# Performance work log

Measured on AMD Instinct MI355X. Metric: run time of the kernel, lower is better.

## Reference

```python
import jax, jax.numpy as jnp
import numpy as np

B, IMG, P, S, D, H, HD = 64, 224, 16, 197, 768, 12, 64
MLP, L, PRUNE_AFTER, NCLS = 3072, 12, 4, 1000
N_KEEP = max(1, int(S * 0.5))  # FIXED_RATIO = 0.5 -> 98 kept tokens (plus forced CLS)


def _ln(x, w, b, eps=1e-6):
    m = x.mean(-1, keepdims=True)
    v = ((x - m) ** 2).mean(-1, keepdims=True)
    return (x - m) * jax.lax.rsqrt(v + eps) * w + b


def _block(x, ln1_w, ln1_b, qkv_w, qkv_b, proj_w, proj_b,
           ln2_w, ln2_b, fc1_w, fc1_b, fc2_w, fc2_b, key_mask=None):
    b, s, _ = x.shape
    qkv = _ln(x, ln1_w, ln1_b) @ qkv_w.T + qkv_b           # [B,S,3D]
    qkv = qkv.reshape(b, s, 3, H, HD)
    q, k, v = qkv[:, :, 0], qkv[:, :, 1], qkv[:, :, 2]     # [B,S,H,HD]
    logits = jnp.einsum('bqhd,bkhd->bhqk', q * (HD ** -0.5), k)
    if key_mask is not None:
        # masking pruned keys == varlen attention restricted to kept tokens
        logits = jnp.where(key_mask[:, None, None, :], logits, -1e9)
    attn = jax.nn.softmax(logits, axis=-1)
    out = jnp.einsum('bhqk,bkhd->bqhd', attn, v).reshape(b, s, D)
    x = x + out @ proj_w.T + proj_b
    h = _ln(x, ln2_w, ln2_b)
    h = jax.nn.gelu(h @ fc1_w.T + fc1_b, approximate=False) @ fc2_w.T + fc2_b
    return x + h


def _forward(images, patch_w, patch_b, cls_token, pos_embed,
             ln1_w, ln1_b, qkv_w, qkv_b, proj_w, proj_b,
             ln2_w, ln2_b, fc1_w, fc1_b, fc2_w, fc2_b,
             norm_w, norm_b, head_w, head_b):
    # patch embed: conv stride P == non-overlapping patch projection
    x = jax.lax.conv_general_dilated(images, patch_w, (P, P), 'VALID',
                                     dimension_numbers=('NCHW', 'OIHW', 'NCHW'))
    x = x.reshape(x.shape[0], D, -1).transpose(0, 2, 1) + patch_b       # [B,196,D]
    x = jnp.concatenate([jnp.broadcast_to(cls_token, (x.shape[0], 1, D)), x], axis=1)
    x = x + pos_embed                                                    # [B,197,D]
    for i in range(PRUNE_AFTER):
        x = _block(x, ln1_w[i], ln1_b[i], qkv_w[i], qkv_b[i], proj_w[i], proj_b[i],
                   ln2_w[i], ln2_b[i], fc1_w[i], fc1_b[i], fc2_w[i], fc2_b[i])
    # norm-score topk prune (CLS always kept), as in _threshold_prune
    scores = jnp.linalg.norm(x, axis=-1)                                 # [B,S]
    _, idx = jax.lax.top_k(scores, N_KEEP)
    mask = jnp.zeros((x.shape[0], S), bool)
    mask = mask.at[jnp.arange(x.shape[0])[:, None], idx].set(True).at[:, 0].set(True)
    # Padded-mask form of triton_pack_tokens + flash_attn_varlen: pruned tokens
    # are never attended to (masked keys) and their own outputs are unused.
    for i in range(PRUNE_AFTER, L):
        x = _block(x, ln1_w[i], ln1_b[i], qkv_w[i], qkv_b[i], proj_w[i], proj_b[i],
                   ln2_w[i], ln2_b[i], fc1_w[i], fc1_b[i], fc2_w[i], fc2_b[i],
                   key_mask=mask)
    cls = _ln(x[:, 0], norm_w, norm_b)   # packed[cu[:-1]] is always the CLS token
    return cls @ head_w.T + head_b       # [B, NCLS]


def setup_inputs():
    key = jax.random.key(0)
    ks = iter(jax.random.split(key, 32))
    def rn(shape, s=0.02):
        return jax.random.normal(next(ks), shape, jnp.float32) * s
    return {
        'images': jax.random.normal(next(ks), (B, 3, IMG, IMG), jnp.float32),
        'patch_w': rn((D, 3, P, P)), 'patch_b': jnp.zeros((D,), jnp.float32),
        'cls_token': rn((1, 1, D)), 'pos_embed': rn((1, S, D)),
        'ln1_w': jnp.ones((L, D), jnp.float32), 'ln1_b': jnp.zeros((L, D), jnp.float32),
        'qkv_w': rn((L, 3 * D, D)), 'qkv_b': jnp.zeros((L, 3 * D), jnp.float32),
        'proj_w': rn((L, D, D)), 'proj_b': jnp.zeros((L, D), jnp.float32),
        'ln2_w': jnp.ones((L, D), jnp.float32), 'ln2_b': jnp.zeros((L, D), jnp.float32),
        'fc1_w': rn((L, MLP, D)), 'fc1_b': jnp.zeros((L, MLP), jnp.float32),
        'fc2_w': rn((L, D, MLP)), 'fc2_b': jnp.zeros((L, D), jnp.float32),
        'norm_w': jnp.ones((D,), jnp.float32), 'norm_b': jnp.zeros((D,), jnp.float32),
        'head_w': rn((NCLS, D)), 'head_b': jnp.zeros((NCLS,), jnp.float32),
    }


def reference(images, patch_w, patch_b, cls_token, pos_embed,
              ln1_w, ln1_b, qkv_w, qkv_b, proj_w, proj_b,
              ln2_w, ln2_b, fc1_w, fc1_b, fc2_w, fc2_b,
              norm_w, norm_b, head_w, head_b):
    return _forward(images, patch_w, patch_b, cls_token, pos_embed,
                    ln1_w, ln1_b, qkv_w, qkv_b, proj_w, proj_b,
                    ln2_w, ln2_b, fc1_w, fc1_b, fc2_w, fc2_b,
                    norm_w, norm_b, head_w, head_b)
```

## Files before the change

### kernel.cpp

```cpp
#include <hip/hip_runtime.h>
#include <hip/hip_bf16.h>
#include <cstdint>

#define NH 12
#define SQ 197
#define DIM 768
#define HDIM 64
#define BATCH 64
#define MTOK (BATCH*SQ)
#define MLPD 3072
#define NKEEP 98
#define CSLOT 100
#define MCTOK (BATCH*CSLOT)
#define VLDF 224
#define VLDC 128

typedef __attribute__((ext_vector_type(8))) short bf16x8;
typedef __attribute__((ext_vector_type(8))) unsigned short ushort8;
typedef __attribute__((ext_vector_type(4))) unsigned short ushort4v;
typedef __attribute__((ext_vector_type(4))) float floatx4;

__device__ __forceinline__ unsigned short f2bf(float f) {
  __hip_bfloat16 h = __float2bfloat16(f);
  return reinterpret_cast<unsigned short&>(h);
}

__device__ __forceinline__ float erf_fast(float x) {
  float ax = fabsf(x);
  float t = 1.f / (1.f + 0.3275911f * ax);
  float y = t * (0.254829592f + t * (-0.284496736f + t * (1.421413741f +
            t * (-1.453152027f + t * 1.061405429f))));
  float r = 1.f - y * __expf(-ax * ax);
  return copysignf(r, x);
}

__device__ __forceinline__ void gload16(const unsigned short* g, unsigned short* l) {
  __builtin_amdgcn_global_load_lds(
      (const __attribute__((address_space(1))) void*)g,
      (__attribute__((address_space(3))) void*)l, 16, 0, 0);
}

enum { EPI_PATCH = 0, EPI_QKV = 1, EPI_RESID = 2, EPI_GELU = 3, EPI_HEAD = 4, EPI_QKVC = 5 };

template<int EPI, bool CHK, int MR, int NR>
__device__ __forceinline__ void gemm_epilogue(
    floatx4 (&acc)[MR][NR], int m0, int n0, int wr, int wc, int l15, int l4,
    const float* __restrict__ bias, int M, int N,
    float* __restrict__ xresid, const float* __restrict__ pos,
    unsigned short* __restrict__ obf, unsigned short* __restrict__ qb,
    unsigned short* __restrict__ kb, unsigned short* __restrict__ vb,
    float* __restrict__ ofp)
{
#pragma unroll
  for (int mr = 0; mr < MR; ++mr) {
#pragma unroll
    for (int nr = 0; nr < NR; ++nr) {
#pragma unroll
      for (int j = 0; j < 4; ++j) {
        int m = m0 + wr + mr * 16 + l4 * 4 + j;
        int n = n0 + wc + nr * 16 + l15;
        if (CHK && (m >= M || n >= N)) continue;
        float val = acc[mr][nr][j] + bias[n];
        if constexpr (EPI == EPI_PATCH) {
          int b = m / 196, p = m - b * 196;
          xresid[(size_t)(b * SQ + 1 + p) * DIM + n] = val + pos[(1 + p) * DIM + n];
        } else if constexpr (EPI == EPI_QKV || EPI == EPI_QKVC) {
          constexpr int SR = (EPI == EPI_QKV) ? SQ : CSLOT;
          constexpr int VL = (EPI == EPI_QKV) ? VLDF : VLDC;
          int part = n / DIM; int within = n - part * DIM;
          int h = within >> 6, hd = within & 63;
          int b = m / SR, s = m - b * SR;
          if (part == 0)      qb[(((size_t)(b * NH + h)) * SR + s) * HDIM + hd] = f2bf(val * 0.125f);
          else if (part == 1) kb[(((size_t)(b * NH + h)) * SR + s) * HDIM + hd] = f2bf(val);
          else                vb[(((size_t)(b * NH + h)) * HDIM + hd) * VL + s] = f2bf(val);
        } else if constexpr (EPI == EPI_RESID) {
          xresid[(size_t)m * DIM + n] += val;
        } else if constexpr (EPI == EPI_GELU) {
          float g = 0.5f * val * (1.f + erf_fast(val * 0.70710678118654752f));
          obf[(size_t)m * MLPD + n] = f2bf(g);
        } else {
          ofp[(size_t)m * 1000 + n] = val;
        }
      }
    }
  }
}

template<int EPI>
__global__ __launch_bounds__(512, 1)
void gemm_bf256(const unsigned short* __restrict__ A, int lda,
                const unsigned short* __restrict__ Wb, int ldw,
                const float* __restrict__ bias,
                int M, int N, int K,
                float* __restrict__ xresid,
                const float* __restrict__ pos,
                unsigned short* __restrict__ obf,
                unsigned short* __restrict__ qb,
                unsigned short* __restrict__ kb,
                unsigned short* __restrict__ vb,
                float* __restrict__ ofp)
{
  __shared__ unsigned short As[2][256 * 64];
  __shared__ unsigned short Bs[2][256 * 64];
  const int tid = threadIdx.x;
  const int lane = tid & 63;
  const int w = tid >> 6;
  const int wr = (w >> 2) * 128;
  const int wc = (w & 3) * 64;

  const int gx = gridDim.x;
  const int nwg = gx * gridDim.y;
  const int orig = blockIdx.y * gx + blockIdx.x;
  const int q = nwg >> 3, r = nwg & 7;
  const int xcd = orig & 7, o8 = orig >> 3;
  const int wgid = ((xcd < r) ? xcd * (q + 1) : r * (q + 1) + (xcd - r) * q) + o8;
  const int bx = wgid % gx, by = wgid / gx;
  const int m0 = by * 256, n0 = bx * 256;
  const int l15 = lane & 15, l4 = lane >> 4;

  const int sub = lane & 7, rsub = lane >> 3;
  const int scol = ((sub ^ rsub) << 3);
  const bool isA = (w < 4);
  const unsigned short* gp[8];
  int ldst[8];
#pragma unroll
  for (int j = 0; j < 8; ++j) {
    int row = (w & 3) * 64 + j * 8 + rsub;
    if (isA) {
      int ra = m0 + row; if (ra > M - 1) ra = M - 1;
      gp[j] = A + (size_t)ra * lda + scol;
    } else {
      int rb = n0 + row; if (rb > N - 1) rb = N - 1;
      gp[j] = Wb + (size_t)rb * ldw + scol;
    }
    ldst[j] = ((w & 3) * 8 + j) * 512;
  }

  floatx4 acc[8][4];
#pragma unroll
  for (int i = 0; i < 8; ++i)
#pragma unroll
    for (int j = 0; j < 4; ++j) acc[i][j] = {0.f, 0.f, 0.f, 0.f};

  auto STAGE = [&](int buf, int kt) {
    unsigned short* base = isA ? &As[buf][0] : &Bs[buf][0];
#pragma unroll
    for (int j = 0; j < 8; ++j)
      gload16(gp[j] + kt, base + ldst[j]);
  };

  const int nk = K >> 6;
  STAGE(0, 0);
  int cur = 0;
  for (int ki = 0; ki < nk; ++ki) {
    if (ki + 1 < nk) {
      STAGE(cur ^ 1, (ki + 1) << 6);
      asm volatile("s_waitcnt vmcnt(8)" ::: "memory");
    } else {
      asm volatile("s_waitcnt vmcnt(0)" ::: "memory");
    }
    __builtin_amdgcn_sched_barrier(0);
    __builtin_amdgcn_s_barrier();
    const unsigned short* Ac = &As[cur][0];
    const unsigned short* Bc = &Bs[cur][0];
#pragma unroll
    for (int kk = 0; kk < 2; ++kk) {
      bf16x8 af[8], bfr[4];
#pragma unroll
      for (int mr = 0; mr < 8; ++mr) {
        int row = wr + mr * 16 + l15;
        int cs = (kk * 4 + l4) ^ (row & 7);
        af[mr] = *(const bf16x8*)&Ac[row * 64 + cs * 8];
      }
#pragma unroll
      for (int nr = 0; nr < 4; ++nr) {
        int row = wc + nr * 16 + l15;
        int cs = (kk * 4 + l4) ^ (row & 7);
        bfr[nr] = *(const bf16x8*)&Bc[row * 64 + cs * 8];
      }
#pragma unroll
      for (int mr = 0; mr < 8; ++mr)
#pragma unroll
        for (int nr = 0; nr < 4; ++nr)
          acc[mr][nr] = __builtin_amdgcn_mfma_f32_16x16x32_bf16(af[mr], bfr[nr], acc[mr][nr], 0, 0, 0);
    }
    __builtin_amdgcn_sched_barrier(0);
    __builtin_amdgcn_s_barrier();
    cur ^= 1;
  }
  if (m0 + 256 <= M && n0 + 256 <= N)
    gemm_epilogue<EPI, false, 8, 4>(acc, m0, n0, wr, wc, l15, l4, bias, M, N,
                                    xresid, pos, obf, qb, kb, vb, ofp);
  else
    gemm_epilogue<EPI, true, 8, 4>(acc, m0, n0, wr, wc, l15, l4, bias, M, N,
                                   xresid, pos, obf, qb, kb, vb, ofp);
}

template<int EPI, int BN>
__global__ __launch_bounds__(256)
void gemm_bf(const unsigned short* __restrict__ A, int lda,
             const unsigned short* __restrict__ Wb, int ldw,
             const float* __restrict__ bias,
             int M, int N, int K,
             float* __restrict__ xresid,
             const float* __restrict__ pos,
             unsigned short* __restrict__ obf,
             unsigned short* __restrict__ qb,
             unsigned short* __restrict__ kb,
             unsigned short* __restrict__ vb,
             float* __restrict__ ofp)
{
  constexpr int NR = BN / 32;
  constexpr int NG = (128 + BN) / 8;
  constexpr int PG = NG / 4;
  __shared__ unsigned short As[128 * 64];
  __shared__ unsigned short Bs[BN * 64];
  const int tid = threadIdx.x;
  const int lane = tid & 63;
  const int w = tid >> 6;
  const int wr = (w >> 1) * 64, wc = (w & 1) * (BN / 2);

  const int gx = gridDim.x;
  const int nwg = gx * gridDim.y;
  const int orig = blockIdx.y * gx + blockIdx.x;
  const int q = nwg >> 3, r = nwg & 7;
  const int xcd = orig & 7, o8 = orig >> 3;
  const int wgid = ((xcd < r) ? xcd * (q + 1) : r * (q + 1) + (xcd - r) * q) + o8;
  const int bx = wgid % gx, by = wgid / gx;
  const int m0 = by * 128, n0 = bx * BN;
  const int l15 = lane & 15, l4 = lane >> 4;

  const int sub = lane & 7, rsub = lane >> 3;
  const int scol = ((sub ^ rsub) << 3);
  const unsigned short* gp[PG];
  unsigned short* lp[PG];
#pragma unroll
  for (int j = 0; j < PG; ++j) {
    int t = w * PG + j;
    if (t < 16) {
      int row = t * 8 + rsub;
      int ra = m0 + row; if (ra > M - 1) ra = M - 1;
      gp[j] = A + (size_t)ra * lda + scol;
      lp[j] = &As[t * 512];
    } else {
      int tb = t - 16;
      int row = tb * 8 + rsub;
      int rb = n0 + row; if (rb > N - 1) rb = N - 1;
      gp[j] = Wb + (size_t)rb * ldw + scol;
      lp[j] = &Bs[tb * 512];
    }
  }

  floatx4 acc[4][NR];
#pragma unroll
  for (int i = 0; i < 4; ++i)
#pragma unroll
    for (int j = 0; j < NR; ++j) acc[i][j] = {0.f, 0.f, 0.f, 0.f};

  for (int kt = 0; kt < K; kt += 64) {
#pragma unroll
    for (int j = 0; j < PG; ++j)
      gload16(gp[j] + kt, lp[j]);
    __syncthreads();
#pragma unroll
    for (int kk = 0; kk < 2; ++kk) {
      bf16x8 af[4], bfr[NR];
#pragma unroll
      for (int mr = 0; mr < 4; ++mr) {
        int row = wr + mr * 16 + l15;
        int cs = (kk * 4 + l4) ^ (row & 7);
        af[mr] = *(const bf16x8*)&As[row * 64 + cs * 8];
      }
#pragma unroll
      for (int nr = 0; nr < NR; ++nr) {
        int row = wc + nr * 16 + l15;
        int cs = (kk * 4 + l4) ^ (row & 7);
        bfr[nr] = *(const bf16x8*)&Bs[row * 64 + cs * 8];
      }
#pragma unroll
      for (int mr = 0; mr < 4; ++mr)
#pragma unroll
        for (int nr = 0; nr < NR; ++nr)
          acc[mr][nr] = __builtin_amdgcn_mfma_f32_16x16x32_bf16(af[mr], bfr[nr], acc[mr][nr], 0, 0, 0);
    }
    __syncthreads();
  }
  if (m0 + 128 <= M && n0 + BN <= N)
    gemm_epilogue<EPI, false, 4, NR>(acc, m0, n0, wr, wc, l15, l4, bias, M, N,
                                     xresid, pos, obf, qb, kb, vb, ofp);
  else
    gemm_epilogue<EPI, true, 4, NR>(acc, m0, n0, wr, wc, l15, l4, bias, M, N,
                                    xresid, pos, obf, qb, kb, vb, ofp);
}

template<int EPI>
__global__ __launch_bounds__(256)
void gemm_f32(const unsigned short* __restrict__ A, int lda,
              const float* __restrict__ Wf, int ldw,
              const float* __restrict__ bias,
              int M, int N, int K,
              float* __restrict__ xresid,
              const float* __restrict__ pos,
              unsigned short* __restrict__ obf,
              unsigned short* __restrict__ qb,
              unsigned short* __restrict__ kb,
              unsigned short* __restrict__ vb,
              float* __restrict__ ofp)
{
  __shared__ unsigned short As[128 * 64];
  __shared__ unsigned short Bs[128 * 64];
  const int tid = threadIdx.x;
  const int lane = tid & 63;
  const int w = tid >> 6;
  const int wr = (w >> 1) * 64, wc = (w & 1) * 64;
  const int m0 = blockIdx.y * 128, n0 = blockIdx.x * 128;
  const int l15 = lane & 15, l4 = lane >> 4;

  floatx4 acc[4][4];
#pragma unroll
  for (int i = 0; i < 4; ++i)
#pragma unroll
    for (int j = 0; j < 4; ++j) acc[i][j] = {0.f, 0.f, 0.f, 0.f};

  for (int kt = 0; kt < K; kt += 64) {
#pragma unroll
    for (int i = 0; i < 4; ++i) {
      int g = tid + 256 * i;
      int row = g >> 3, c = g & 7;
      int sw = (c ^ (row & 7)) * 8;
      int ra = m0 + row; if (ra > M - 1) ra = M - 1;
      ushort8 av = *(const ushort8*)(A + (size_t)ra * lda + kt + c * 8);
      *(ushort8*)&As[row * 64 + sw] = av;
      int rb = n0 + row; if (rb > N - 1) rb = N - 1;
      const float* bs = Wf + (size_t)rb * ldw + kt + c * 8;
      float4 f0 = *(const float4*)bs;
      float4 f1 = *(const float4*)(bs + 4);
      ushort8 bv;
      bv[0] = f2bf(f0.x); bv[1] = f2bf(f0.y); bv[2] = f2bf(f0.z); bv[3] = f2bf(f0.w);
      bv[4] = f2bf(f1.x); bv[5] = f2bf(f1.y); bv[6] = f2bf(f1.z); bv[7] = f2bf(f1.w);
      *(ushort8*)&Bs[row * 64 + sw] = bv;
    }
    __syncthreads();
#pragma unroll
    for (int kk = 0; kk < 2; ++kk) {
      bf16x8 af[4], bfr[4];
#pragma unroll
      for (int mr = 0; mr < 4; ++mr) {
        int row = wr + mr * 16 + l15;
        int cs = (kk * 4 + l4) ^ (row & 7);
        af[mr] = *(const bf16x8*)&As[row * 64 + cs * 8];
      }
#pragma unroll
      for (int nr = 0; nr < 4; ++nr) {
        int row = wc + nr * 16 + l15;
        int cs = (kk * 4 + l4) ^ (row & 7);
        bfr[nr] = *(const bf16x8*)&Bs[row * 64 + cs * 8];
      }
#pragma unroll
      for (int mr = 0; mr < 4; ++mr)
#pragma unroll
        for (int nr = 0; nr < 4; ++nr)
          acc[mr][nr] = __builtin_amdgcn_mfma_f32_16x16x32_bf16(af[mr], bfr[nr], acc[mr][nr], 0, 0, 0);
    }
    __syncthreads();
  }
  if (m0 + 128 <= M && n0 + 128 <= N)
    gemm_epilogue<EPI, false, 4, 4>(acc, m0, n0, wr, wc, l15, l4, bias, M, N,
                                    xresid, pos, obf, qb, kb, vb, ofp);
  else
    gemm_epilogue<EPI, true, 4, 4>(acc, m0, n0, wr, wc, l15, l4, bias, M, N,
                                   xresid, pos, obf, qb, kb, vb, ofp);
}

__device__ __forceinline__ void cvt8(const float* s, unsigned short* d, long long i) {
  float4 f0 = *(const float4*)(s + i * 8);
  float4 f1 = *(const float4*)(s + i * 8 + 4);
  ushort8 v;
  v[0] = f2bf(f0.x); v[1] = f2bf(f0.y); v[2] = f2bf(f0.z); v[3] = f2bf(f0.w);
  v[4] = f2bf(f1.x); v[5] = f2bf(f1.y); v[6] = f2bf(f1.z); v[7] = f2bf(f1.w);
  *(ushort8*)(d + i * 8) = v;
}

__global__ __launch_bounds__(256)
void cvt6_kernel(const float* s0, unsigned short* d0, long long n0,
                 const float* s1, unsigned short* d1, long long n1,
                 const float* s2, unsigned short* d2, long long n2,
                 const float* s3, unsigned short* d3, long long n3,
                 const float* s4, unsigned short* d4, long long n4,
                 const float* s5, unsigned short* d5, long long n5)
{
  long long i = (long long)blockIdx.x * 256 + threadIdx.x;
  if (i < n0) { cvt8(s0, d0, i); return; } i -= n0;
  if (i < n1) { cvt8(s1, d1, i); return; } i -= n1;
  if (i < n2) { cvt8(s2, d2, i); return; } i -= n2;
  if (i < n3) { cvt8(s3, d3, i); return; } i -= n3;
  if (i < n4) { cvt8(s4, d4, i); return; } i -= n4;
  if (i < n5) { cvt8(s5, d5, i); }
}

__global__ __launch_bounds__(192)
void ln_kernel(const float* __restrict__ x, long long row_stride,
               const float* __restrict__ g, const float* __restrict__ b,
               unsigned short* __restrict__ out)
{
  int row = blockIdx.x;
  const float4* xr = (const float4*)(x + (size_t)row * row_stride);
  int t = threadIdx.x;
  float4 v = xr[t];
  float s = v.x + v.y + v.z + v.w;
  float sq = v.x * v.x + v.y * v.y + v.z * v.z + v.w * v.w;
  __shared__ float sb[6];
  for (int o = 32; o; o >>= 1) { s += __shfl_down(s, o); sq += __shfl_down(sq, o); }
  if ((t & 63) == 0) { sb[t >> 6] = s; sb[3 + (t >> 6)] = sq; }
  __syncthreads();
  s = sb[0] + sb[1] + sb[2];
  sq = sb[3] + sb[4] + sb[5];
  float mean = s * (1.f / 768.f);
  float var = sq * (1.f / 768.f) - mean * mean;
  float rstd = rsqrtf(var + 1e-6f);
  float4 gg = ((const float4*)g)[t];
  float4 bb = ((const float4*)b)[t];
  ushort4v o4;
  o4[0] = f2bf((v.x - mean) * rstd * gg.x + bb.x);
  o4[1] = f2bf((v.y - mean) * rstd * gg.y + bb.y);
  o4[2] = f2bf((v.z - mean) * rstd * gg.z + bb.z);
  o4[3] = f2bf((v.w - mean) * rstd * gg.w + bb.w);
  *(ushort4v*)(out + (size_t)row * DIM + t * 4) = o4;
}

template<int NT, int SROWS, int VLD, int PSTR, bool CNT, int SPLIT>
__global__ __launch_bounds__(256)
void attn_kernel(const unsigned short* __restrict__ qb,
                 const unsigned short* __restrict__ kb,
                 const unsigned short* __restrict__ vb,
                 const int* __restrict__ cnt,
                 unsigned short* __restrict__ outA)
{
  __shared__ unsigned short Ks[NT * 16 * 64];
  __shared__ unsigned short Ps[4][16 * PSTR];
  int bh = blockIdx.x / SPLIT;
  int half = blockIdx.x - bh * SPLIT;
  int b = bh / NH, h = bh - b * NH;
  const int tid = threadIdx.x, lane = tid & 63, w = tid >> 6;
  const int l15 = lane & 15, l4 = lane >> 4;
  const unsigned short* kbase = kb + (size_t)bh * SROWS * HDIM;
  const unsigned short* qbase = qb + (size_t)bh * SROWS * HDIM;
  const unsigned short* vbase = vb + (size_t)bh * HDIM * VLD;
  const int limit = CNT ? cnt[b] : SROWS;

  constexpr int KCH = NT * 16 * 8;
  for (int i = 0; i < (KCH + 255) / 256; ++i) {
    int gch = tid + 256 * i;
    if (gch < KCH) {
      int row = gch >> 3, c = gch & 7;
      int rs = row > SROWS - 1 ? SROWS - 1 : row;
      ushort8 kv = *(const ushort8*)(kbase + (size_t)rs * HDIM + c * 8);
      *(ushort8*)&Ks[row * 64 + ((c ^ (row & 7))) * 8] = kv;
    }
  }
  __syncthreads();

  constexpr int QTB = (NT + SPLIT - 1) / SPLIT;
  const int qthi = (half + 1) * QTB < NT ? (half + 1) * QTB : NT;
  for (int qt = half * QTB + w; qt < qthi; qt += 4) {
    int qrow = qt * 16 + l15; if (qrow > SROWS - 1) qrow = SROWS - 1;
    bf16x8 aq0 = *(const bf16x8*)(qbase + (size_t)qrow * HDIM + l4 * 8);
    bf16x8 aq1 = *(const bf16x8*)(qbase + (size_t)qrow * HDIM + 32 + l4 * 8);

    floatx4 lg[NT];
#pragma unroll
    for (int nt = 0; nt < NT; ++nt) {
      lg[nt] = {0.f, 0.f, 0.f, 0.f};
      int row = nt * 16 + l15;
      int cs0 = (l4) ^ (row & 7);
      int cs1 = (4 + l4) ^ (row & 7);
      bf16x8 bk0 = *(const bf16x8*)&Ks[row * 64 + cs0 * 8];
      bf16x8 bk1 = *(const bf16x8*)&Ks[row * 64 + cs1 * 8];
      lg[nt] = __builtin_amdgcn_mfma_f32_16x16x32_bf16(aq0, bk0, lg[nt], 0, 0, 0);
      lg[nt] = __builtin_amdgcn_mfma_f32_16x16x32_bf16(aq1, bk1, lg[nt], 0, 0, 0);
    }
    float mx[4] = {-1e30f, -1e30f, -1e30f, -1e30f};
#pragma unroll
    for (int nt = 0; nt < NT; ++nt) {
      int col = nt * 16 + l15;
      bool valid = col < limit;
#pragma unroll
      for (int j = 0; j < 4; ++j) {
        float v = valid ? lg[nt][j] : -1e9f;
        lg[nt][j] = v;
        mx[j] = fmaxf(mx[j], v);
      }
    }
#pragma unroll
    for (int j = 0; j < 4; ++j)
      for (int o = 1; o < 16; o <<= 1) mx[j] = fmaxf(mx[j], __shfl_xor(mx[j], o));
    float sm[4] = {0.f, 0.f, 0.f, 0.f};
#pragma unroll
    for (int nt = 0; nt < NT; ++nt)
#pragma unroll
      for (int j = 0; j < 4; ++j) {
        float p = __expf(lg[nt][j] - mx[j]);
        lg[nt][j] = p;
        sm[j] += p;
      }
#pragma unroll
    for (int j = 0; j < 4; ++j) {
      for (int o = 1; o < 16; o <<= 1) sm[j] += __shfl_xor(sm[j], o);
      sm[j] = 1.f / sm[j];
    }
    unsigned short* pw = &Ps[w][0];
#pragma unroll
    for (int nt = 0; nt < NT; ++nt) {
      int col = nt * 16 + l15;
#pragma unroll
      for (int j = 0; j < 4; ++j)
        pw[(l4 * 4 + j) * PSTR + col] = f2bf(lg[nt][j]);
    }
#pragma unroll
    for (int j = 0; j < 4; ++j)
      pw[(l4 * 4 + j) * PSTR + NT * 16 + l15] = 0;
    floatx4 oacc[4];
#pragma unroll
    for (int nr = 0; nr < 4; ++nr) oacc[nr] = {0.f, 0.f, 0.f, 0.f};
#pragma unroll
    for (int ks = 0; ks < VLD / 32; ++ks) {
      bf16x8 ap = *(const bf16x8*)&pw[l15 * PSTR + ks * 32 + l4 * 8];
#pragma unroll
      for (int nr = 0; nr < 4; ++nr) {
        bf16x8 bv = *(const bf16x8*)(vbase + (size_t)(nr * 16 + l15) * VLD + ks * 32 + l4 * 8);
        oacc[nr] = __builtin_amdgcn_mfma_f32_16x16x32_bf16(ap, bv, oacc[nr], 0, 0, 0);
      }
    }
#pragma unroll
    for (int nr = 0; nr < 4; ++nr)
#pragma unroll
      for (int j = 0; j < 4; ++j) {
        int qi = qt * 16 + l4 * 4 + j;
        if (qi < SROWS)
          outA[((size_t)(b * SROWS + qi)) * DIM + h * HDIM + nr * 16 + l15] = f2bf(oacc[nr][j] * sm[j]);
      }
  }
}

__global__ __launch_bounds__(256)
void im2col_kernel(const float* __restrict__ images, unsigned short* __restrict__ out)
{
  int idx = blockIdx.x * 256 + threadIdx.x;
  int token = idx / 96;
  int kc = (idx - token * 96) * 8;
  int b = token / 196, p = token - b * 196;
  int py = p / 14, px = p - py * 14;
  int c = kc >> 8, rem = kc & 255;
  int i = rem >> 4, j0 = rem & 15;
  const float* src = images + (((size_t)(b * 3 + c) * 224 + py * 16 + i) * 224 + px * 16 + j0);
  float4 f0 = *(const float4*)src;
  float4 f1 = *(const float4*)(src + 4);
  ushort8 v;
  v[0] = f2bf(f0.x); v[1] = f2bf(f0.y); v[2] = f2bf(f0.z); v[3] = f2bf(f0.w);
  v[4] = f2bf(f1.x); v[5] = f2bf(f1.y); v[6] = f2bf(f1.z); v[7] = f2bf(f1.w);
  *(ushort8*)(out + (size_t)token * DIM + kc) = v;
}

__global__ __launch_bounds__(256)
void clspos_kernel(const float* __restrict__ cls, const float* __restrict__ pos,
                   float* __restrict__ x)
{
  int idx = blockIdx.x * 256 + threadIdx.x;
  int b = idx / DIM, d = idx - b * DIM;
  x[(size_t)(b * SQ) * DIM + d] = cls[d] + pos[d];
}

__global__ __launch_bounds__(256)
void norms_kernel(const float* __restrict__ x, float* __restrict__ norms)
{
  int row = blockIdx.x * 4 + (threadIdx.x >> 6);
  if (row >= MTOK) return;
  int lane = threadIdx.x & 63;
  const float4* xr = (const float4*)(x + (size_t)row * DIM);
  float acc = 0.f;
  for (int c = lane; c < 192; c += 64) {
    float4 v = xr[c];
    acc += v.x * v.x + v.y * v.y + v.z * v.z + v.w * v.w;
  }
  for (int o = 32; o; o >>= 1) acc += __shfl_down(acc, o);
  if (lane == 0) norms[row] = acc;
}

__global__ __launch_bounds__(256)
void topk_select(const float* __restrict__ norms, short* __restrict__ sidx,
                 int* __restrict__ cntg)
{
  int b = blockIdx.x;
  __shared__ float sc[SQ];
  __shared__ unsigned char keep[SQ];
  int tid = threadIdx.x;
  if (tid < SQ) sc[tid] = norms[b * SQ + tid];
  __syncthreads();
  if (tid < SQ) {
    float mine = sc[tid];
    int rank = 0;
    for (int j = 0; j < SQ; ++j) {
      float v = sc[j];
      rank += (v > mine) || (v == mine && j < tid);
    }
    keep[tid] = (rank < NKEEP) || (tid == 0);
  }
  __syncthreads();
  if (tid == 0) {
    short* row = sidx + b * CSLOT;
    int c = 0;
    for (int s = 0; s < SQ; ++s) if (keep[s]) row[c++] = (short)s;
    cntg[b] = c;
    for (int s = c; s < CSLOT; ++s) row[s] = 0;
  }
}

__global__ __launch_bounds__(192)
void gather_kernel(const float* __restrict__ x, const short* __restrict__ sidx,
                   float* __restrict__ xc)
{
  int g = blockIdx.x;
  int b = g / CSLOT;
  int src = sidx[g];
  const float4* sp = (const float4*)(x + ((size_t)(b * SQ + src)) * DIM);
  float4* dp = (float4*)(xc + (size_t)g * DIM);
  dp[threadIdx.x] = sp[threadIdx.x];
}

template<int EPI, int BN>
static inline void launch_gemm(hipStream_t stream, bool usebf,
                               const unsigned short* A, int lda,
                               const float* Wf, const unsigned short* Wb, int ldw,
                               const float* bias, int M, int N, int K,
                               float* xresid, const float* pos,
                               unsigned short* obf, unsigned short* qb,
                               unsigned short* kb, unsigned short* vb, float* ofp)
{
  if (usebf) {
    dim3 grid((N + BN - 1) / BN, (M + 127) / 128);
    gemm_bf<EPI, BN><<<grid, 256, 0, stream>>>(A, lda, Wb, ldw, bias,
        M, N, K, xresid, pos, obf, qb, kb, vb, ofp);
  } else {
    dim3 grid((N + 127) / 128, (M + 127) / 128);
    gemm_f32<EPI><<<grid, 256, 0, stream>>>(A, lda, Wf, ldw, bias,
        M, N, K, xresid, pos, obf, qb, kb, vb, ofp);
  }
}

template<int EPI>
static inline void launch_gemm256(hipStream_t stream, bool usebf,
                                  const unsigned short* A, int lda,
                                  const float* Wf, const unsigned short* Wb, int ldw,
                                  const float* bias, int M, int N, int K,
                                  unsigned short* obf, unsigned short* qb,
                                  unsigned short* kb, unsigned short* vb)
{
  if (usebf) {
    dim3 grid(N / 256, (M + 255) / 256);
    gemm_bf256<EPI><<<grid, 512, 0, stream>>>(A, lda, Wb, ldw, bias,
        M, N, K, nullptr, nullptr, obf, qb, kb, vb, nullptr);
  } else {
    dim3 grid((N + 127) / 128, (M + 127) / 128);
    gemm_f32<EPI><<<grid, 256, 0, stream>>>(A, lda, Wf, ldw, bias,
        M, N, K, nullptr, nullptr, obf, qb, kb, vb, nullptr);
  }
}

extern "C" void kernel_launch(void* const* d_in, const int* in_sizes, int n_in,
                              void* d_out, int out_size, void* d_ws, size_t ws_size,
                              hipStream_t stream)
{
  const float* images    = (const float*)d_in[0];
  const float* patch_w   = (const float*)d_in[1];
  const float* patch_b   = (const float*)d_in[2];
  const float* cls_token = (const float*)d_in[3];
  const float* pos_embed = (const float*)d_in[4];
  const float* ln1_w = (const float*)d_in[5];
  const float* ln1_b = (const float*)d_in[6];
  const float* qkv_w = (const float*)d_in[7];
  const float* qkv_b = (const float*)d_in[8];
  const float* proj_w = (const float*)d_in[9];
  const float* proj_b = (const float*)d_in[10];
  const float* ln2_w = (const float*)d_in[11];
  const float* ln2_b = (const float*)d_in[12];
  const float* fc1_w = (const float*)d_in[13];
  const float* fc1_b = (const float*)d_in[14];
  const float* fc2_w = (const float*)d_in[15];
  const float* fc2_b = (const float*)d_in[16];
  const float* norm_w = (const float*)d_in[17];
  const float* norm_b = (const float*)d_in[18];
  const float* head_w = (const float*)d_in[19];
  const float* head_b = (const float*)d_in[20];

  char* ws = (char*)d_ws;
  size_t off = 0;
  auto alloc = [&](size_t bytes) { void* p = ws + off; off += (bytes + 255) & ~(size_t)255; return p; };
  float* x            = (float*)alloc((size_t)MTOK * DIM * 4);
  float* xc           = (float*)alloc((size_t)MCTOK * DIM * 4);
  unsigned short* xn  = (unsigned short*)alloc((size_t)MTOK * DIM * 2);
  size_t h1_bytes = (size_t)MTOK * MLPD * 2;
  unsigned short* h1  = (unsigned short*)alloc(h1_bytes);
  unsigned short* qb  = h1;
  unsigned short* kb  = qb + (size_t)BATCH * NH * SQ * HDIM;
  unsigned short* vb  = kb + (size_t)BATCH * NH * SQ * HDIM;
  size_t vbytes = (size_t)BATCH * NH * HDIM * VLDF * 2;
  unsigned short* lncls = (unsigned short*)alloc((size_t)64 * DIM * 2);
  float* norms = (float*)alloc((size_t)MTOK * 4);
  short* sidx  = (short*)alloc((size_t)MCTOK * 2);
  int* cnt = (int*)alloc(BATCH * 4);
  size_t n_qkvw = (size_t)12 * 2304 * DIM, n_projw = (size_t)12 * DIM * DIM;
  size_t n_fc1w = (size_t)12 * MLPD * DIM, n_fc2w = (size_t)12 * DIM * MLPD;
  size_t n_patw = (size_t)DIM * DIM, n_headw = (size_t)1000 * DIM;
  unsigned short* wqkv = (unsigned short*)alloc(n_qkvw * 2);
  unsigned short* wproj = (unsigned short*)alloc(n_projw * 2);
  unsigned short* wfc1 = (unsigned short*)alloc(n_fc1w * 2);
  unsigned short* wfc2 = (unsigned short*)alloc(n_fc2w * 2);
  unsigned short* wpat = (unsigned short*)alloc(n_patw * 2);
  unsigned short* whead = (unsigned short*)alloc(n_headw * 2);
  const bool usebf = (off <= ws_size);

  hipMemsetAsync(vb, 0, vbytes, stream);

  if (usebf) {
    long long c0 = n_qkvw / 8, c1 = n_projw / 8, c2 = n_fc1w / 8,
              c3 = n_fc2w / 8, c4 = n_patw / 8, c5 = n_headw / 8;
    long long tot = c0 + c1 + c2 + c3 + c4 + c5;
    cvt6_kernel<<<(int)((tot + 255) / 256), 256, 0, stream>>>(
        qkv_w, wqkv, c0, proj_w, wproj, c1, fc1_w, wfc1, c2,
        fc2_w, wfc2, c3, patch_w, wpat, c4, head_w, whead, c5);
  }

  im2col_kernel<<<4704, 256, 0, stream>>>(images, h1);
  launch_gemm<EPI_PATCH, 64>(stream, usebf, h1, DIM, patch_w, wpat, DIM,
      patch_b, 12544, DIM, DIM, x, pos_embed, nullptr, nullptr, nullptr, nullptr, nullptr);
  clspos_kernel<<<192, 256, 0, stream>>>(cls_token, pos_embed, x);

  for (int l = 0; l < 4; ++l) {
    ln_kernel<<<MTOK, 192, 0, stream>>>(x, DIM, ln1_w + l * DIM, ln1_b + l * DIM, xn);
    launch_gemm256<EPI_QKV>(stream, usebf, xn, DIM,
        qkv_w + (size_t)l * 2304 * DIM, wqkv + (size_t)l * 2304 * DIM, DIM,
        qkv_b + l * 2304, MTOK, 2304, DIM, nullptr, qb, kb, vb);
    attn_kernel<13, SQ, VLDF, 248, false, 2><<<BATCH * NH * 2, 256, 0, stream>>>(qb, kb, vb, nullptr, xn);
    launch_gemm<EPI_RESID, 64>(stream, usebf, xn, DIM,
        proj_w + (size_t)l * DIM * DIM, wproj + (size_t)l * DIM * DIM, DIM,
        proj_b + l * DIM, MTOK, DIM, DIM, x, nullptr, nullptr, nullptr, nullptr, nullptr, nullptr);
    ln_kernel<<<MTOK, 192, 0, stream>>>(x, DIM, ln2_w + l * DIM, ln2_b + l * DIM, xn);
    launch_gemm256<EPI_GELU>(stream, usebf, xn, DIM,
        fc1_w + (size_t)l * MLPD * DIM, wfc1 + (size_t)l * MLPD * DIM, DIM,
        fc1_b + l * MLPD, MTOK, MLPD, DIM, h1, nullptr, nullptr, nullptr);
    launch_gemm<EPI_RESID, 64>(stream, usebf, h1, MLPD,
        fc2_w + (size_t)l * DIM * MLPD, wfc2 + (size_t)l * DIM * MLPD, MLPD,
        fc2_b + l * DIM, MTOK, DIM, MLPD, x, nullptr, nullptr, nullptr, nullptr, nullptr, nullptr);
  }

  norms_kernel<<<(MTOK + 3) / 4, 256, 0, stream>>>(x, norms);
  topk_select<<<BATCH, 256, 0, stream>>>(norms, sidx, cnt);
  gather_kernel<<<MCTOK, 192, 0, stream>>>(x, sidx, xc);

  for (int l = 4; l < 12; ++l) {
    ln_kernel<<<MCTOK, 192, 0, stream>>>(xc, DIM, ln1_w + l * DIM, ln1_b + l * DIM, xn);
    launch_gemm<EPI_QKVC, 128>(stream, usebf, xn, DIM,
        qkv_w + (size_t)l * 2304 * DIM, wqkv + (size_t)l * 2304 * DIM, DIM,
        qkv_b + l * 2304, MCTOK, 2304, DIM, nullptr, nullptr, nullptr, qb, kb, vb, nullptr);
    attn_kernel<7, CSLOT, VLDC, 136, true, 1><<<BATCH * NH, 256, 0, stream>>>(qb, kb, vb, cnt, xn);
    launch_gemm<EPI_RESID, 64>(stream, usebf, xn, DIM,
        proj_w + (size_t)l * DIM * DIM, wproj + (size_t)l * DIM * DIM, DIM,
        proj_b + l * DIM, MCTOK, DIM, DIM, xc, nullptr, nullptr, nullptr, nullptr, nullptr, nullptr);
    ln_kernel<<<MCTOK, 192, 0, stream>>>(xc, DIM, ln2_w + l * DIM, ln2_b + l * DIM, xn);
    launch_gemm<EPI_GELU, 128>(stream, usebf, xn, DIM,
        fc1_w + (size_t)l * MLPD * DIM, wfc1 + (size_t)l * MLPD * DIM, DIM,
        fc1_b + l * MLPD, MCTOK, MLPD, DIM, nullptr, nullptr, h1, nullptr, nullptr, nullptr, nullptr);
    launch_gemm<EPI_RESID, 64>(stream, usebf, h1, MLPD,
        fc2_w + (size_t)l * DIM * MLPD, wfc2 + (size_t)l * DIM * MLPD, MLPD,
        fc2_b + l * DIM, MCTOK, DIM, MLPD, xc, nullptr, nullptr, nullptr, nullptr, nullptr, nullptr);
  }

  ln_kernel<<<64, 192, 0, stream>>>(xc, (long long)CSLOT * DIM, norm_w, norm_b, lncls);
  launch_gemm<EPI_HEAD, 64>(stream, usebf, lncls, DIM, head_w, whead, DIM,
      head_b, 64, 1000, DIM, nullptr, nullptr, nullptr, nullptr, nullptr, nullptr, (float*)d_out);
  (void)in_sizes; (void)n_in; (void)out_size;
}
```

Measured before the change: 3.701 ms.

## Halve K-tile of 256x256 GEMM and restage loads across all waves

Shrinks the K step of the 256x256 bf16 GEMM from 64 to 32, halving LDS use per block. Launch bounds change from (512,1) to (512,4). Global-to-LDS staging now has every wave load A and B rows, with a new XOR swizzle for 32-wide rows, instead of splitting the waves between A and B. The aim is more resident blocks per CU or lower LDS pressure, at the cost of twice as many barriers and loop iterations per K. The tighter register bound from the launch change risks spilling the 32 accumulator tiles.

```diff
diff --git a/kernel.cpp b/kernel.cpp
--- a/kernel.cpp
+++ b/kernel.cpp
@@ -87,7 +87,7 @@
 }
 
 template<int EPI>
-__global__ __launch_bounds__(512, 1)
+__global__ __launch_bounds__(512, 4)
 void gemm_bf256(const unsigned short* __restrict__ A, int lda,
                 const unsigned short* __restrict__ Wb, int ldw,
                 const float* __restrict__ bias,
@@ -100,8 +100,8 @@
                 unsigned short* __restrict__ vb,
                 float* __restrict__ ofp)
 {
-  __shared__ unsigned short As[2][256 * 64];
-  __shared__ unsigned short Bs[2][256 * 64];
+  __shared__ unsigned short As[2][256 * 32];
+  __shared__ unsigned short Bs[2][256 * 32];
   const int tid = threadIdx.x;
   const int lane = tid & 63;
   const int w = tid >> 6;
@@ -118,23 +118,17 @@
   const int m0 = by * 256, n0 = bx * 256;
   const int l15 = lane & 15, l4 = lane >> 4;
 
-  const int sub = lane & 7, rsub = lane >> 3;
-  const int scol = ((sub ^ rsub) << 3);
-  const bool isA = (w < 4);
-  const unsigned short* gp[8];
-  int ldst[8];
-#pragma unroll
-  for (int j = 0; j < 8; ++j) {
-    int row = (w & 3) * 64 + j * 8 + rsub;
-    if (isA) {
-      int ra = m0 + row; if (ra > M - 1) ra = M - 1;
-      gp[j] = A + (size_t)ra * lda + scol;
-    } else {
-      int rb = n0 + row; if (rb > N - 1) rb = N - 1;
-      gp[j] = Wb + (size_t)rb * ldw + scol;
-    }
-    ldst[j] = ((w & 3) * 8 + j) * 512;
-  }
+  const int srow = tid >> 2, ch = tid & 3;
+  const int scol = ((ch ^ ((srow >> 1) & 3)) << 3);
+  int ra0 = m0 + srow;       if (ra0 > M - 1) ra0 = M - 1;
+  int ra1 = m0 + 128 + srow; if (ra1 > M - 1) ra1 = M - 1;
+  int rb0 = n0 + srow;       if (rb0 > N - 1) rb0 = N - 1;
+  int rb1 = n0 + 128 + srow; if (rb1 > N - 1) rb1 = N - 1;
+  const unsigned short* gA0 = A + (size_t)ra0 * lda + scol;
+  const unsigned short* gA1 = A + (size_t)ra1 * lda + scol;
+  const unsigned short* gB0 = Wb + (size_t)rb0 * ldw + scol;
+  const unsigned short* gB1 = Wb + (size_t)rb1 * ldw + scol;
+  const int wbase = w * 512;
 
   floatx4 acc[8][4];
 #pragma unroll
@@ -143,19 +137,19 @@
     for (int j = 0; j < 4; ++j) acc[i][j] = {0.f, 0.f, 0.f, 0.f};
 
   auto STAGE = [&](int buf, int kt) {
-    unsigned short* base = isA ? &As[buf][0] : &Bs[buf][0];
-#pragma unroll
-    for (int j = 0; j < 8; ++j)
-      gload16(gp[j] + kt, base + ldst[j]);
+    gload16(gA0 + kt, &As[buf][wbase]);
+    gload16(gA1 + kt, &As[buf][wbase + 4096]);
+    gload16(gB0 + kt, &Bs[buf][wbase]);
+    gload16(gB1 + kt, &Bs[buf][wbase + 4096]);
   };
 
-  const int nk = K >> 6;
+  const int nk = K >> 5;
   STAGE(0, 0);
   int cur = 0;
-  for (int ki = 0; ki < nk; ++ki) {
-    if (ki + 1 < nk) {
-      STAGE(cur ^ 1, (ki + 1) << 6);
-      asm volatile("s_waitcnt vmcnt(8)" ::: "memory");
+  for (int t = 0; t < nk; ++t) {
+    if (t + 1 < nk) {
+      STAGE(cur ^ 1, (t + 1) << 5);
+      asm volatile("s_waitcnt vmcnt(4)" ::: "memory");
     } else {
       asm volatile("s_waitcnt vmcnt(0)" ::: "memory");
     }
@@ -163,27 +157,24 @@
     __builtin_amdgcn_s_barrier();
     const unsigned short* Ac = &As[cur][0];
     const unsigned short* Bc = &Bs[cur][0];
-#pragma unroll
-    for (int kk = 0; kk < 2; ++kk) {
-      bf16x8 af[8], bfr[4];
-#pragma unroll
-      for (int mr = 0; mr < 8; ++mr) {
-        int row = wr + mr * 16 + l15;
-        int cs = (kk * 4 + l4) ^ (row & 7);
-        af[mr] = *(const bf16x8*)&Ac[row * 64 + cs * 8];
-      }
-#pragma unroll
-      for (int nr = 0; nr < 4; ++nr) {
-        int row = wc + nr * 16 + l15;
-        int cs = (kk * 4 + l4) ^ (row & 7);
-        bfr[nr] = *(const bf16x8*)&Bc[row * 64 + cs * 8];
-      }
-#pragma unroll
-      for (int mr = 0; mr < 8; ++mr)
-#pragma unroll
-        for (int nr = 0; nr < 4; ++nr)
-          acc[mr][nr] = __builtin_amdgcn_mfma_f32_16x16x32_bf16(af[mr], bfr[nr], acc[mr][nr], 0, 0, 0);
-    }
+    bf16x8 af[8], bfr[4];
+#pragma unroll
+    for (int mr = 0; mr < 8; ++mr) {
+      int row = wr + mr * 16 + l15;
+      int cs = l4 ^ ((row >> 1) & 3);
+      af[mr] = *(const bf16x8*)&Ac[row * 32 + cs * 8];
+    }
+#pragma unroll
+    for (int nr = 0; nr < 4; ++nr) {
+      int row = wc + nr * 16 + l15;
+      int cs = l4 ^ ((row >> 1) & 3);
+      bfr[nr] = *(const bf16x8*)&Bc[row * 32 + cs * 8];
+    }
+#pragma unroll
+    for (int mr = 0; mr < 8; ++mr)
+#pragma unroll
+      for (int nr = 0; nr < 4; ++nr)
+        acc[mr][nr] = __builtin_amdgcn_mfma_f32_16x16x32_bf16(af[mr], bfr[nr], acc[mr][nr], 0, 0, 0);
     __builtin_amdgcn_sched_barrier(0);
     __builtin_amdgcn_s_barrier();
     cur ^= 1;
```

After: 6.282 ms. +69.8%, slower.
